# Performance work log

Hardware: AMD Instinct MI355X
Metric: run time of the kernel (lower is better)

Reference implementation:

```python
import jax, jax.numpy as jnp
import numpy as np

N, T = 512, 48
VOCAB, EMBED, HIDDEN, IMG_DIM = 32000, 1024, 1024, 4096


def setup_inputs() -> dict:
    key = jax.random.key(0)
    ks = jax.random.split(key, 12)
    s = 0.02
    return {
        "questions": jax.random.randint(ks[0], (N, T), 0, VOCAB, dtype=jnp.int32),
        "img_features": jax.random.normal(ks[1], (N, IMG_DIM), dtype=jnp.float32),
        "emb": jax.random.normal(ks[2], (VOCAB, EMBED), dtype=jnp.float32) * s,
        "W_img": jax.random.normal(ks[3], (HIDDEN, IMG_DIM), dtype=jnp.float32) * s,
        "b_img": jnp.zeros((HIDDEN,), dtype=jnp.float32),
        "W_ih": jax.random.normal(ks[4], (4 * HIDDEN, EMBED), dtype=jnp.float32) * s,
        "W_hh": jax.random.normal(ks[5], (4 * HIDDEN, HIDDEN), dtype=jnp.float32) * s,
        "b_ih": jnp.zeros((4 * HIDDEN,), dtype=jnp.float32),
        "b_hh": jnp.zeros((4 * HIDDEN,), dtype=jnp.float32),
        "W_out": jax.random.normal(ks[6], (VOCAB, HIDDEN), dtype=jnp.float32) * s,
        "b_out": jnp.zeros((VOCAB,), dtype=jnp.float32),
        "first_words": 1,
    }


def reference(questions, img_features, emb, W_img, b_img, W_ih, W_hh, b_ih, b_hh,
              W_out, b_out, first_words):
    H = W_hh.shape[1]
    n = questions.shape[0]
    emb_q = emb[questions].transpose(1, 0, 2)          # [T, N, E]
    emb_i = img_features @ W_img.T + b_img             # [N, H]
    if first_words:
        seq = jnp.concatenate([emb_i[None], emb_q], axis=0)   # [T+1, N, E]
    else:
        seq = jnp.concatenate([emb_q, emb_i[None]], axis=0)

    def cell(carry, x_t):
        h, c = carry
        gates = x_t @ W_ih.T + b_ih + h @ W_hh.T + b_hh   # [N, 4H]
        i, f, g, o = jnp.split(gates, 4, axis=-1)          # torch LSTMCell gate order
        i, f, o = jax.nn.sigmoid(i), jax.nn.sigmoid(f), jax.nn.sigmoid(o)
        g = jnp.tanh(g)
        c = f * c + i * g
        h = o * jnp.tanh(c)
        return (h, c), h

    h0 = jnp.zeros((n, H), dtype=seq.dtype)
    (_, _), hs = jax.lax.scan(cell, (h0, h0), seq)     # hs: [T+1, N, H]
    hidden_states = hs.transpose(1, 0, 2)              # [N, T+1, H]
    output = hidden_states[:, -1, :] @ W_out.T + b_out  # [N, vocab]
    return output, hidden_states
```

## Files before the change

### kernel.cpp

```cpp
#include <hip/hip_runtime.h>
#include <hip/hip_bf16.h>
#include <stdint.h>

typedef __bf16 bf16_t;
typedef __attribute__((ext_vector_type(8))) __bf16 bf16x8;
typedef __attribute__((ext_vector_type(4))) __bf16 bf16x4;
typedef __attribute__((ext_vector_type(4))) float f32x4;
#define LL long long

__device__ __forceinline__ void gl_lds16(const bf16_t* g, bf16_t* s) {
  __builtin_amdgcn_global_load_lds(
      (const __attribute__((address_space(1))) void*)g,
      (__attribute__((address_space(3))) void*)s, 16, 0, 0);
}

__device__ __forceinline__ float sigm(float x) {
  return 1.0f / (1.0f + __expf(-x));
}
__device__ __forceinline__ float tanh_s(float x) {
  float e = __expf(-2.0f * fabsf(x));
  float t = (1.0f - e) / (1.0f + e);
  return copysignf(t, x);
}

template<int BM, int OUTBF>
__global__ __launch_bounds__(256, 2)
void gemm_bt(const bf16_t* __restrict__ A, const bf16_t* __restrict__ B,
             const float* __restrict__ bias,
             bf16_t* __restrict__ Cb, float* __restrict__ Cf,
             int N, int K, const int* __restrict__ fw, LL off0, LL off1) {
  __shared__ bf16_t lds_a[BM * 32];
  __shared__ bf16_t lds_b[128 * 32];
  const int tid = threadIdx.x;
  const int w = tid >> 6, l = tid & 63;
  const LL m0 = (LL)blockIdx.x * BM;
  const LL n0 = (LL)blockIdx.y * 128;
  constexpr int MI = BM / 32;
  const int wm = w & 1, wn = w >> 1;
  f32x4 acc[MI][4] = {};

  const int srow = l >> 2;
  const int scol = (l & 3) * 8;

  for (int kt = 0; kt < K; kt += 32) {
    for (int c = w; c < BM / 16; c += 4)
      gl_lds16(A + (m0 + c * 16 + srow) * K + kt + scol, &lds_a[c * 512]);
#pragma unroll
    for (int j = 0; j < 2; ++j) {
      int c = w * 2 + j;
      gl_lds16(B + (n0 + c * 16 + srow) * K + kt + scol, &lds_b[c * 512]);
    }
    __syncthreads();
    const int fr = l & 15, fk = (l >> 4) * 8;
    bf16x8 af[MI], bfr[4];
#pragma unroll
    for (int i = 0; i < MI; ++i)
      af[i] = *(const bf16x8*)&lds_a[(wm * (BM / 2) + i * 16 + fr) * 32 + fk];
#pragma unroll
    for (int j = 0; j < 4; ++j)
      bfr[j] = *(const bf16x8*)&lds_b[(wn * 64 + j * 16 + fr) * 32 + fk];
#pragma unroll
    for (int i = 0; i < MI; ++i)
#pragma unroll
      for (int j = 0; j < 4; ++j)
        acc[i][j] = __builtin_amdgcn_mfma_f32_16x16x32_bf16(af[i], bfr[j],
                                                            acc[i][j], 0, 0, 0);
    __syncthreads();
  }

  const LL coff = (fw[0] ? off1 : off0);
  const int er = (l >> 4) * 4, ec = l & 15;
#pragma unroll
  for (int i = 0; i < MI; ++i) {
#pragma unroll
    for (int j = 0; j < 4; ++j) {
      LL mrow = m0 + wm * (BM / 2) + i * 16 + er;
      LL ncol = n0 + wn * 64 + j * 16 + ec;
      float bs = bias[ncol];
#pragma unroll
      for (int r = 0; r < 4; ++r) {
        float v = acc[i][j][r] + bs;
        if (OUTBF) Cb[coff + (mrow + r) * N + ncol] = (bf16_t)v;
        else       Cf[(mrow + r) * N + ncol] = v;
      }
    }
  }
}

__global__ __launch_bounds__(256, 2)
void lstm_step(const bf16_t* __restrict__ h_in, const bf16_t* __restrict__ Whh,
               const bf16_t* __restrict__ Gt, float* __restrict__ c,
               bf16_t* __restrict__ h_out, float* __restrict__ hid, int t) {
  __shared__ bf16_t lds_a[2][64 * 32];
  __shared__ bf16_t lds_b[2][64 * 32];
  __shared__ float lds_ex[64 * 64];
  const int tid = threadIdx.x;
  const int w = tid >> 6, l = tid & 63;
  const int bid = blockIdx.x + (blockIdx.y << 3);
  const int g = bid & 7, q = bid >> 3;
  const int m0 = (q & 7) * 64;
  const int n0 = ((g << 3) | (q >> 3)) * 64;
  const int wm = w & 1, wn = w >> 1;
  f32x4 acc[2][2] = {};
  const int srow = l >> 2, scol = (l & 3) * 8;
  const int fr = l & 15, fk = (l >> 4) * 8;

  auto stage = [&](int buf, int kt) {
    gl_lds16(h_in + (LL)(m0 + w * 16 + srow) * 1024 + kt + scol,
             &lds_a[buf][w * 512]);
    gl_lds16(Whh + (LL)(n0 + w * 16 + srow) * 1024 + kt + scol,
             &lds_b[buf][w * 512]);
  };
  auto compute = [&](int buf) {
    bf16x8 af[2], bfr[2];
#pragma unroll
    for (int i = 0; i < 2; ++i)
      af[i] = *(const bf16x8*)&lds_a[buf][(wm * 32 + i * 16 + fr) * 32 + fk];
#pragma unroll
    for (int j = 0; j < 2; ++j)
      bfr[j] = *(const bf16x8*)&lds_b[buf][(wn * 32 + j * 16 + fr) * 32 + fk];
#pragma unroll
    for (int i = 0; i < 2; ++i)
#pragma unroll
      for (int j = 0; j < 2; ++j)
        acc[i][j] = __builtin_amdgcn_mfma_f32_16x16x32_bf16(af[i], bfr[j],
                                                            acc[i][j], 0, 0, 0);
  };

  stage(0, 0);
  __syncthreads();
#pragma unroll 1
  for (int kt = 0; kt < 1024; kt += 64) {
    stage(1, kt + 32);
    compute(0);
    __syncthreads();
    if (kt + 64 < 1024) stage(0, kt + 64);
    compute(1);
    __syncthreads();
  }

  const int er = (l >> 4) * 4, ec = l & 15;
#pragma unroll
  for (int i = 0; i < 2; ++i)
#pragma unroll
    for (int j = 0; j < 2; ++j)
#pragma unroll
      for (int r = 0; r < 4; ++r)
        lds_ex[(wm * 32 + i * 16 + er + r) * 64 + wn * 32 + j * 16 + ec] =
            acc[i][j][r];
  __syncthreads();

  for (int cidx = tid; cidx < 1024; cidx += 256) {
    int ml = cidx >> 4, jl = cidx & 15;
    int m = m0 + ml;
    int j = (n0 >> 2) + jl;
    float4 ge = *(const float4*)&lds_ex[ml * 64 + jl * 4];
    bf16x4 g4 = *(const bf16x4*)(Gt + (LL)m * 4096 + n0 + jl * 4);
    float gi = ge.x + (float)g4[0];
    float gf = ge.y + (float)g4[1];
    float gg = ge.z + (float)g4[2];
    float go = ge.w + (float)g4[3];
    float iv = sigm(gi), fv = sigm(gf), gv = tanh_s(gg), ov = sigm(go);
    LL cij = (LL)m * 1024 + j;
    float cn = fv * c[cij] + iv * gv;
    float hn = ov * tanh_s(cn);
    c[cij] = cn;
    h_out[cij] = (bf16_t)hn;
    hid[((LL)m * 49 + t) * 1024 + j] = hn;
  }
}

__global__ __launch_bounds__(256)
void cvt_f2b(const float* __restrict__ src, bf16_t* __restrict__ dst, LL n4) {
  LL i = (LL)blockIdx.x * blockDim.x + threadIdx.x;
  LL stride = (LL)gridDim.x * blockDim.x;
  for (; i < n4; i += stride) {
    float4 v = *(const float4*)(src + i * 4);
    bf16x4 o;
    o[0] = (bf16_t)v.x; o[1] = (bf16_t)v.y; o[2] = (bf16_t)v.z; o[3] = (bf16_t)v.w;
    *(bf16x4*)(dst + i * 4) = o;
  }
}

__global__ __launch_bounds__(256)
void permute_w(const float* __restrict__ W, bf16_t* __restrict__ Wp) {
  int p = blockIdx.x;
  int r = (p & 3) * 1024 + (p >> 2);
  float4 v = *(const float4*)(W + (LL)r * 1024 + threadIdx.x * 4);
  bf16x4 o;
  o[0] = (bf16_t)v.x; o[1] = (bf16_t)v.y; o[2] = (bf16_t)v.z; o[3] = (bf16_t)v.w;
  *(bf16x4*)(Wp + (LL)p * 1024 + threadIdx.x * 4) = o;
}

__global__ __launch_bounds__(256)
void bias_comb(const float* __restrict__ bih, const float* __restrict__ bhh,
               float* __restrict__ bp) {
  int p = blockIdx.x * blockDim.x + threadIdx.x;
  int r = (p & 3) * 1024 + (p >> 2);
  bp[p] = bih[r] + bhh[r];
}

__global__ __launch_bounds__(256)
void gather_emb(const int* __restrict__ q, const float* __restrict__ emb,
                bf16_t* __restrict__ Xb, const int* __restrict__ fw) {
  int b = blockIdx.x;
  int tq = b >> 9;
  int n = b & 511;
  int slot = fw[0] ? tq + 1 : tq;
  int row = q[n * 48 + tq];
  float4 v = *(const float4*)(emb + (LL)row * 1024 + threadIdx.x * 4);
  bf16x4 o;
  o[0] = (bf16_t)v.x; o[1] = (bf16_t)v.y; o[2] = (bf16_t)v.z; o[3] = (bf16_t)v.w;
  *(bf16x4*)(Xb + ((LL)slot * 512 + n) * 1024 + threadIdx.x * 4) = o;
}

extern "C" void kernel_launch(void* const* d_in, const int* in_sizes, int n_in,
                              void* d_out, int out_size, void* d_ws,
                              size_t ws_size, hipStream_t stream) {
  const int*   questions = (const int*)  d_in[0];
  const float* img       = (const float*)d_in[1];
  const float* emb       = (const float*)d_in[2];
  const float* W_img     = (const float*)d_in[3];
  const float* b_img     = (const float*)d_in[4];
  const float* W_ih      = (const float*)d_in[5];
  const float* W_hh      = (const float*)d_in[6];
  const float* b_ih      = (const float*)d_in[7];
  const float* b_hh      = (const float*)d_in[8];
  const float* W_out     = (const float*)d_in[9];
  const float* b_out     = (const float*)d_in[10];
  const int*   fw        = (const int*)  d_in[11];

  char* ws = (char*)d_ws;
  size_t off = 0;
  auto alloc = [&](size_t bytes) {
    char* p = ws + off;
    off += (bytes + 255) & ~(size_t)255;
    return p;
  };
  bf16_t* Xb    = (bf16_t*)alloc((size_t)49 * 512 * 1024 * 2);
  bf16_t* G     = (bf16_t*)alloc((size_t)49 * 512 * 4096 * 2);
  bf16_t* Wp_ih = (bf16_t*)alloc((size_t)4096 * 1024 * 2);
  bf16_t* Wp_hh = (bf16_t*)alloc((size_t)4096 * 1024 * 2);
  bf16_t* Woutb = (bf16_t*)alloc((size_t)32000 * 1024 * 2);
  bf16_t* Wimgb = (bf16_t*)alloc((size_t)1024 * 4096 * 2);
  bf16_t* imgb  = (bf16_t*)alloc((size_t)512 * 4096 * 2);
  float*  biasp = (float*) alloc((size_t)4096 * 4);
  bf16_t* h0    = (bf16_t*)alloc((size_t)512 * 1024 * 2);
  bf16_t* h1    = (bf16_t*)alloc((size_t)512 * 1024 * 2);
  float*  cbuf  = (float*) alloc((size_t)512 * 1024 * 4);

  float* out0 = (float*)d_out;
  float* hid  = out0 + (size_t)512 * 32000;

  hipMemsetAsync(h0, 0, (size_t)512 * 1024 * 2, stream);
  hipMemsetAsync(cbuf, 0, (size_t)512 * 1024 * 4, stream);

  cvt_f2b<<<dim3(2048), dim3(256), 0, stream>>>(W_out, Woutb, (LL)32000 * 1024 / 4);
  cvt_f2b<<<dim3(1024), dim3(256), 0, stream>>>(W_img, Wimgb, (LL)1024 * 4096 / 4);
  cvt_f2b<<<dim3(512),  dim3(256), 0, stream>>>(img,   imgb,  (LL)512 * 4096 / 4);
  permute_w<<<dim3(4096), dim3(256), 0, stream>>>(W_ih, Wp_ih);
  permute_w<<<dim3(4096), dim3(256), 0, stream>>>(W_hh, Wp_hh);
  bias_comb<<<dim3(16), dim3(256), 0, stream>>>(b_ih, b_hh, biasp);
  gather_emb<<<dim3(48 * 512), dim3(256), 0, stream>>>(questions, emb, Xb, fw);

  gemm_bt<64, 1><<<dim3(8, 8), dim3(256), 0, stream>>>(
      imgb, Wimgb, b_img, Xb, nullptr, 1024, 4096, fw,
      (LL)48 * 512 * 1024, (LL)0);

  gemm_bt<128, 1><<<dim3(196, 32), dim3(256), 0, stream>>>(
      Xb, Wp_ih, biasp, G, nullptr, 4096, 1024, fw, 0, 0);

  for (int t = 0; t < 49; ++t) {
    const bf16_t* hin = (t & 1) ? h1 : h0;
    bf16_t* hout = (t & 1) ? h0 : h1;
    lstm_step<<<dim3(8, 64), dim3(256), 0, stream>>>(
        hin, Wp_hh, G + (LL)t * 512 * 4096, cbuf, hout, hid, t);
  }

  gemm_bt<128, 0><<<dim3(4, 250), dim3(256), 0, stream>>>(
      h1, Woutb, b_out, nullptr, out0, 32000, 1024, fw, 0, 0);
}
```

Before: 1.604 ms.

## Double-buffer GEMM LDS, widen LSTM step K-tile, prefetch gate and cell inputs

The generic bf16 GEMM now uses two LDS buffers, so loading the next K tile overlaps the MFMA work on the current one instead of serialising load and compute. The per-timestep LSTM kernel doubles its K tile from 32 to 64, which halves the number of loop iterations and barriers. It also loads the precomputed input-gate values and the previous cell state into registers before the recurrent GEMM starts, hiding that global latency behind the matmul. The cost is more LDS per block and more registers, which may lower occupancy.

```diff
diff --git a/kernel.cpp b/kernel.cpp
--- a/kernel.cpp
+++ b/kernel.cpp
@@ -29,8 +29,8 @@
              const float* __restrict__ bias,
              bf16_t* __restrict__ Cb, float* __restrict__ Cf,
              int N, int K, const int* __restrict__ fw, LL off0, LL off1) {
-  __shared__ bf16_t lds_a[BM * 32];
-  __shared__ bf16_t lds_b[128 * 32];
+  __shared__ bf16_t lds_a[2][BM * 32];
+  __shared__ bf16_t lds_b[2][128 * 32];
   const int tid = threadIdx.x;
   const int w = tid >> 6, l = tid & 63;
   const LL m0 = (LL)blockIdx.x * BM;
@@ -41,30 +41,42 @@
 
   const int srow = l >> 2;
   const int scol = (l & 3) * 8;
-
-  for (int kt = 0; kt < K; kt += 32) {
+  const int fr = l & 15, fk = (l >> 4) * 8;
+
+  auto stage = [&](int buf, int kt) {
     for (int c = w; c < BM / 16; c += 4)
-      gl_lds16(A + (m0 + c * 16 + srow) * K + kt + scol, &lds_a[c * 512]);
+      gl_lds16(A + (m0 + c * 16 + srow) * K + kt + scol, &lds_a[buf][c * 512]);
 #pragma unroll
     for (int j = 0; j < 2; ++j) {
       int c = w * 2 + j;
-      gl_lds16(B + (n0 + c * 16 + srow) * K + kt + scol, &lds_b[c * 512]);
+      gl_lds16(B + (n0 + c * 16 + srow) * K + kt + scol, &lds_b[buf][c * 512]);
     }
-    __syncthreads();
-    const int fr = l & 15, fk = (l >> 4) * 8;
+  };
+  auto compute = [&](int buf) {
     bf16x8 af[MI], bfr[4];
 #pragma unroll
     for (int i = 0; i < MI; ++i)
-      af[i] = *(const bf16x8*)&lds_a[(wm * (BM / 2) + i * 16 + fr) * 32 + fk];
+      af[i] = *(const bf16x8*)&lds_a[buf][(wm * (BM / 2) + i * 16 + fr) * 32 + fk];
 #pragma unroll
     for (int j = 0; j < 4; ++j)
-      bfr[j] = *(const bf16x8*)&lds_b[(wn * 64 + j * 16 + fr) * 32 + fk];
+      bfr[j] = *(const bf16x8*)&lds_b[buf][(wn * 64 + j * 16 + fr) * 32 + fk];
 #pragma unroll
     for (int i = 0; i < MI; ++i)
 #pragma unroll
       for (int j = 0; j < 4; ++j)
         acc[i][j] = __builtin_amdgcn_mfma_f32_16x16x32_bf16(af[i], bfr[j],
                                                             acc[i][j], 0, 0, 0);
+  };
+
+  stage(0, 0);
+  __syncthreads();
+#pragma unroll 1
+  for (int kt = 0; kt < K; kt += 64) {
+    stage(1, kt + 32);
+    compute(0);
+    __syncthreads();
+    if (kt + 64 < K) stage(0, kt + 64);
+    compute(1);
     __syncthreads();
   }
 
@@ -91,8 +103,8 @@
 void lstm_step(const bf16_t* __restrict__ h_in, const bf16_t* __restrict__ Whh,
                const bf16_t* __restrict__ Gt, float* __restrict__ c,
                bf16_t* __restrict__ h_out, float* __restrict__ hid, int t) {
-  __shared__ bf16_t lds_a[2][64 * 32];
-  __shared__ bf16_t lds_b[2][64 * 32];
+  __shared__ bf16_t lds_a[2][64 * 64];
+  __shared__ bf16_t lds_b[2][64 * 64];
   __shared__ float lds_ex[64 * 64];
   const int tid = threadIdx.x;
   const int w = tid >> 6, l = tid & 63;
@@ -102,39 +114,58 @@
   const int n0 = ((g << 3) | (q >> 3)) * 64;
   const int wm = w & 1, wn = w >> 1;
   f32x4 acc[2][2] = {};
-  const int srow = l >> 2, scol = (l & 3) * 8;
+  const int srow = l >> 3, scol = (l & 7) * 8;
   const int fr = l & 15, fk = (l >> 4) * 8;
 
+  bf16x4 g4p[4];
+  float cvp[4];
+#pragma unroll
+  for (int u = 0; u < 4; ++u) {
+    int cidx = tid + u * 256;
+    int ml = cidx >> 4, jl = cidx & 15;
+    g4p[u] = *(const bf16x4*)(Gt + (LL)(m0 + ml) * 4096 + n0 + jl * 4);
+    cvp[u] = c[(LL)(m0 + ml) * 1024 + (n0 >> 2) + jl];
+  }
+
   auto stage = [&](int buf, int kt) {
-    gl_lds16(h_in + (LL)(m0 + w * 16 + srow) * 1024 + kt + scol,
-             &lds_a[buf][w * 512]);
-    gl_lds16(Whh + (LL)(n0 + w * 16 + srow) * 1024 + kt + scol,
-             &lds_b[buf][w * 512]);
+#pragma unroll
+    for (int j = 0; j < 2; ++j) {
+      int ch = w * 2 + j;
+      gl_lds16(h_in + (LL)(m0 + ch * 8 + srow) * 1024 + kt + scol,
+               &lds_a[buf][ch * 512]);
+      gl_lds16(Whh + (LL)(n0 + ch * 8 + srow) * 1024 + kt + scol,
+               &lds_b[buf][ch * 512]);
+    }
   };
   auto compute = [&](int buf) {
-    bf16x8 af[2], bfr[2];
-#pragma unroll
-    for (int i = 0; i < 2; ++i)
-      af[i] = *(const bf16x8*)&lds_a[buf][(wm * 32 + i * 16 + fr) * 32 + fk];
-#pragma unroll
-    for (int j = 0; j < 2; ++j)
-      bfr[j] = *(const bf16x8*)&lds_b[buf][(wn * 32 + j * 16 + fr) * 32 + fk];
-#pragma unroll
-    for (int i = 0; i < 2; ++i)
+#pragma unroll
+    for (int ks = 0; ks < 2; ++ks) {
+      bf16x8 af[2], bfr[2];
+#pragma unroll
+      for (int i = 0; i < 2; ++i)
+        af[i] = *(const bf16x8*)
+            &lds_a[buf][(wm * 32 + i * 16 + fr) * 64 + ks * 32 + fk];
 #pragma unroll
       for (int j = 0; j < 2; ++j)
-        acc[i][j] = __builtin_amdgcn_mfma_f32_16x16x32_bf16(af[i], bfr[j],
-                                                            acc[i][j], 0, 0, 0);
+        bfr[j] = *(const bf16x8*)
+            &lds_b[buf][(wn * 32 + j * 16 + fr) * 64 + ks * 32 + fk];
+#pragma unroll
+      for (int i = 0; i < 2; ++i)
+#pragma unroll
+        for (int j = 0; j < 2; ++j)
+          acc[i][j] = __builtin_amdgcn_mfma_f32_16x16x32_bf16(af[i], bfr[j],
+                                                              acc[i][j], 0, 0, 0);
+    }
   };
 
   stage(0, 0);
   __syncthreads();
 #pragma unroll 1
-  for (int kt = 0; kt < 1024; kt += 64) {
-    stage(1, kt + 32);
+  for (int kt = 0; kt < 1024; kt += 128) {
+    stage(1, kt + 64);
     compute(0);
     __syncthreads();
-    if (kt + 64 < 1024) stage(0, kt + 64);
+    if (kt + 128 < 1024) stage(0, kt + 128);
     compute(1);
     __syncthreads();
   }
@@ -150,19 +181,20 @@
             acc[i][j][r];
   __syncthreads();
 
-  for (int cidx = tid; cidx < 1024; cidx += 256) {
+#pragma unroll
+  for (int u = 0; u < 4; ++u) {
+    int cidx = tid + u * 256;
     int ml = cidx >> 4, jl = cidx & 15;
     int m = m0 + ml;
     int j = (n0 >> 2) + jl;
     float4 ge = *(const float4*)&lds_ex[ml * 64 + jl * 4];
-    bf16x4 g4 = *(const bf16x4*)(Gt + (LL)m * 4096 + n0 + jl * 4);
-    float gi = ge.x + (float)g4[0];
-    float gf = ge.y + (float)g4[1];
-    float gg = ge.z + (float)g4[2];
-    float go = ge.w + (float)g4[3];
+    float gi = ge.x + (float)g4p[u][0];
+    float gf = ge.y + (float)g4p[u][1];
+    float gg = ge.z + (float)g4p[u][2];
+    float go = ge.w + (float)g4p[u][3];
     float iv = sigm(gi), fv = sigm(gf), gv = tanh_s(gg), ov = sigm(go);
     LL cij = (LL)m * 1024 + j;
-    float cn = fv * c[cij] + iv * gv;
+    float cn = fv * cvp[u] + iv * gv;
     float hn = ov * tanh_s(cn);
     c[cij] = cn;
     h_out[cij] = (bf16_t)hn;
```

Result: slower. 1.659 ms (+3.4%).
